# Performance work log

Hardware: AMD Instinct MI355X
Metric: run time of the kernel (lower is better)

## Reference

```python
import jax, jax.numpy as jnp
import numpy as np

HEIGHT, WIDTH = 480, 640
IN_CHANNEL, OUT_CHANNEL, FILTER = 6, 32, 3
B, N = 8, 16384
X_COL, Y_COL, P_COL = 1, 2, 3


def setup_inputs() -> dict:
    key = jax.random.key(0)
    k1, k2, k3, k4 = jax.random.split(key, 4)
    xytp = jax.random.uniform(k1, (B, N, 4), dtype=jnp.float32)
    features = jax.random.normal(k2, (B, N, IN_CHANNEL), dtype=jnp.float32)
    fan_in = FILTER * FILTER * (IN_CHANNEL + 2)
    W = jax.random.normal(k3, (FILTER, FILTER, IN_CHANNEL + 2, OUT_CHANNEL), dtype=jnp.float32) / jnp.sqrt(jnp.float32(fan_in))
    bias = jax.random.normal(k4, (OUT_CHANNEL,), dtype=jnp.float32) * 0.05
    return {"xytp": xytp, "features": features, "W": W, "bias": bias}


def reference(xytp, features, W, bias):
    Bc, Nc = xytp.shape[:2]
    # polarity channels: [pos, neg] concatenated with extra features -> Cin = in_channel + 2
    p = xytp[..., P_COL:P_COL + 1]
    feat = jnp.concatenate([p, 1.0 - p, features], axis=-1)  # [B, N, Cin]
    # event2image: round normalized coords to integer pixel grid (values in [0, H] / [0, W])
    yy = jnp.round(xytp[..., Y_COL] * HEIGHT).astype(jnp.int32)  # [B, N]
    xx = jnp.round(xytp[..., X_COL] * WIDTH).astype(jnp.int32)   # [B, N]
    H1, W1 = HEIGHT + 1, WIDTH + 1
    Cin = feat.shape[-1]
    bidx = jnp.broadcast_to(jnp.arange(Bc)[:, None], (Bc, Nc))
    # scn.InputLayer(mode=3): sum features at duplicate coordinates -> dense scatter-add
    grid = jnp.zeros((Bc, H1, W1, Cin), feat.dtype).at[bidx, yy, xx].add(feat)
    # SubmanifoldConvolution: inactive sites hold zero features, so a dense SAME conv
    # computes the identical gather+GEMM+scatter result at every active site.
    out_grid = jax.lax.conv_general_dilated(
        grid, W, window_strides=(1, 1), padding='SAME',
        dimension_numbers=('NHWC', 'HWIO', 'NHWC')) + bias
    # scn.OutputLayer: each input event reads the feature at its (b, y, x) site
    return out_grid[bidx, yy, xx]  # [B, N, out_channel]
```

## Files before the change

### kernel.cpp

```cpp
#include <hip/hip_runtime.h>
#include <hip/hip_bf16.h>

#define HEIGHT 480
#define WIDTH  640
#define IN_CH  6
#define CIN    8
#define COUT   32
#define BATCH  8
#define NPTS   16384
#define NPTOT  (BATCH * NPTS)
#define GH 483
#define GW 643
#define NCELLS ((size_t)BATCH * GH * GW)
#define NWORDS 77644

__device__ __forceinline__ size_t cell_idx(int b, int gy, int gx) {
    return ((size_t)b * GH + gy) * GW + gx;
}

__device__ __forceinline__ void point_cell(const float4 q, int point,
                                           int& b, int& gy, int& gx) {
    gy = (int)rintf(q.z * (float)HEIGHT) + 1;
    gx = (int)rintf(q.y * (float)WIDTH) + 1;
    b  = point >> 14;
}

__global__ void zero_masks_kernel(uint4* __restrict__ m4, int n4) {
    int i = blockIdx.x * blockDim.x + threadIdx.x;
    if (i < n4) m4[i] = make_uint4(0u, 0u, 0u, 0u);
}

__global__ void count_kernel(const float4* __restrict__ xytp,
                             unsigned int* __restrict__ occ,
                             unsigned int* __restrict__ multi,
                             float* __restrict__ grid) {
    int point = blockIdx.x * blockDim.x + threadIdx.x;
    if (point >= NPTOT) return;
    float4 q = xytp[point];
    int b, gy, gx;
    point_cell(q, point, b, gy, gx);
    size_t ci = cell_idx(b, gy, gx);
    unsigned int word = (unsigned int)(ci >> 5);
    unsigned int bit  = 1u << (ci & 31);
    unsigned int old = atomicOr(&occ[word], bit);
    if (old & bit) {
        atomicOr(&multi[word], bit);
        float* cell = grid + (ci << 3);
        const float4 z = make_float4(0.f, 0.f, 0.f, 0.f);
        *(float4*)(cell)     = z;
        *(float4*)(cell + 4) = z;
    }
}

__global__ void write_kernel(const float4* __restrict__ xytp,
                             const float*  __restrict__ feats,
                             const unsigned int* __restrict__ multi,
                             float* __restrict__ grid) {
    int point = blockIdx.x * blockDim.x + threadIdx.x;
    if (point >= NPTOT) return;
    float4 q = xytp[point];
    int b, gy, gx;
    point_cell(q, point, b, gy, gx);
    size_t ci = cell_idx(b, gy, gx);

    const float* f = feats + (size_t)point * IN_CH;
    float v0 = q.w, v1 = 1.0f - q.w;
    float f0 = f[0], f1 = f[1], f2 = f[2], f3 = f[3], f4 = f[4], f5 = f[5];

    unsigned int word = (unsigned int)(ci >> 5);
    unsigned int bit  = 1u << (ci & 31);

    float* cell = grid + (ci << 3);
    if (!(multi[word] & bit)) {
        *(float4*)(cell)     = make_float4(v0, v1, f0, f1);
        *(float4*)(cell + 4) = make_float4(f2, f3, f4, f5);
    } else {
        unsafeAtomicAdd(cell + 0, v0);
        unsafeAtomicAdd(cell + 1, v1);
        unsafeAtomicAdd(cell + 2, f0);
        unsafeAtomicAdd(cell + 3, f1);
        unsafeAtomicAdd(cell + 4, f2);
        unsafeAtomicAdd(cell + 5, f3);
        unsafeAtomicAdd(cell + 6, f4);
        unsafeAtomicAdd(cell + 7, f5);
    }
}

__global__ void __launch_bounds__(256)
conv_gather_kernel(const float4* __restrict__ xytp,
                   const float*  __restrict__ grid,
                   const unsigned int* __restrict__ occ,
                   const float*  __restrict__ W,
                   const float*  __restrict__ bias,
                   float* __restrict__ out) {
    int tid = blockIdx.x * blockDim.x + threadIdx.x;
    if (tid >= NPTOT * 2) return;
    int point = tid >> 1;
    int sub   = tid & 1;

    float4 q = xytp[point];
    int b, gy, gx;
    point_cell(q, point, b, gy, gx);
    size_t center  = cell_idx(b, gy, gx);
    size_t base_ci = center - GW - 1;

    unsigned int occ9 = 0;
#pragma unroll
    for (int ky = 0; ky < 3; ++ky) {
        size_t ci_row = base_ci + (size_t)ky * GW;
        size_t word = ci_row >> 5;
        int sh = (int)(ci_row & 31);
        unsigned long long two =
            (((unsigned long long)occ[word + 1]) << 32) | occ[word];
        occ9 |= ((unsigned int)(two >> sh) & 7u) << (ky * 3);
    }

    float4 g0[5], g1[5];
#pragma unroll
    for (int k = 0; k < 9; ++k) {
        if ((k & 1) == sub) {
            if (occ9 & (1u << k)) {
                size_t ci = base_ci + (size_t)(k / 3) * GW + (k % 3);
                const float* cell = grid + (ci << 3);
                g0[k >> 1] = *(const float4*)(cell);
                g1[k >> 1] = *(const float4*)(cell + 4);
            }
        }
    }

    float acc[COUT];
#pragma unroll
    for (int c = 0; c < COUT; ++c) acc[c] = sub ? 0.0f : bias[c];

#pragma unroll
    for (int k = 0; k < 9; ++k) {
        if ((k & 1) == sub) {
            if (occ9 & (1u << k)) {
                float4 a = g0[k >> 1], d = g1[k >> 1];
                float gv[CIN] = {a.x, a.y, a.z, a.w, d.x, d.y, d.z, d.w};
                const float* wp = W + k * CIN * COUT;
#pragma unroll
                for (int ci2 = 0; ci2 < CIN; ++ci2) {
#pragma unroll
                    for (int c = 0; c < COUT; ++c) {
                        acc[c] = fmaf(gv[ci2], wp[ci2 * COUT + c], acc[c]);
                    }
                }
            }
        }
    }

    float res[16];
#pragma unroll
    for (int c = 0; c < 16; ++c) {
        float mine  = sub ? acc[16 + c] : acc[c];
        float other = sub ? acc[c]      : acc[16 + c];
        res[c] = mine + __shfl_xor(other, 1);
    }

    float* o = out + (size_t)point * COUT + sub * 16;
#pragma unroll
    for (int c = 0; c < 16; c += 4) {
        *(float4*)(o + c) = make_float4(res[c], res[c + 1], res[c + 2], res[c + 3]);
    }
}

extern "C" void kernel_launch(void* const* d_in, const int* in_sizes, int n_in,
                              void* d_out, int out_size, void* d_ws, size_t ws_size,
                              hipStream_t stream) {
    const float4* xytp  = (const float4*)d_in[0];
    const float*  feats = (const float*)d_in[1];
    const float*  W     = (const float*)d_in[2];
    const float*  bias  = (const float*)d_in[3];
    float* out = (float*)d_out;

    float* grid = (float*)d_ws;
    const size_t grid_bytes = NCELLS * CIN * sizeof(float);
    unsigned int* occ   = (unsigned int*)((char*)d_ws + grid_bytes);
    unsigned int* multi = occ + NWORDS;
    (void)ws_size;

    const int blk = 256;
    const int nblk_pts = (NPTOT + blk - 1) / blk;

    const int n4 = (2 * NWORDS) / 4;
    zero_masks_kernel<<<(n4 + blk - 1) / blk, blk, 0, stream>>>((uint4*)occ, n4);

    count_kernel<<<nblk_pts, blk, 0, stream>>>(xytp, occ, multi, grid);

    write_kernel<<<nblk_pts, blk, 0, stream>>>(xytp, feats, multi, grid);

    conv_gather_kernel<<<nblk_pts * 2, blk, 0, stream>>>(xytp, grid, occ, W, bias, out);
}
```

Before: 45.98 us.

## Store scatter grid as packed bf16 and process two points per thread

The dense scatter grid now stores each cell's 8 input channels as packed bf16 in one 16-byte uint4 instead of 32 bytes of fp32. This halves the bytes written by the scatter and read by the 3x3 gather, and duplicate cells are summed with a CAS loop on bf16 pairs. The count and write kernels also handle two points per thread. The cost is reduced feature precision, since sums are rounded to bf16 at each step, which may exceed the accuracy tolerance. CAS loops on contended cells are also slower than native float atomics.

```diff
diff --git a/kernel.cpp b/kernel.cpp
--- a/kernel.cpp
+++ b/kernel.cpp
@@ -25,6 +25,27 @@
     b  = point >> 14;
 }
 
+__device__ __forceinline__ unsigned int pack_bf16x2(float a, float b) {
+    union { __hip_bfloat162 h; unsigned int u; } cv;
+    cv.h = __float22bfloat162_rn(make_float2(a, b));
+    return cv.u;
+}
+__device__ __forceinline__ float bflo(unsigned int u) {
+    return __uint_as_float(u << 16);
+}
+__device__ __forceinline__ float bfhi(unsigned int u) {
+    return __uint_as_float(u & 0xffff0000u);
+}
+
+__device__ __forceinline__ void cas_add_bf16x2(unsigned int* addr, float a, float b) {
+    unsigned int oldv = *addr, assumed;
+    do {
+        assumed = oldv;
+        unsigned int nv = pack_bf16x2(bflo(assumed) + a, bfhi(assumed) + b);
+        oldv = atomicCAS(addr, assumed, nv);
+    } while (oldv != assumed);
+}
+
 __global__ void zero_masks_kernel(uint4* __restrict__ m4, int n4) {
     int i = blockIdx.x * blockDim.x + threadIdx.x;
     if (i < n4) m4[i] = make_uint4(0u, 0u, 0u, 0u);
@@ -33,62 +54,58 @@
 __global__ void count_kernel(const float4* __restrict__ xytp,
                              unsigned int* __restrict__ occ,
                              unsigned int* __restrict__ multi,
-                             float* __restrict__ grid) {
-    int point = blockIdx.x * blockDim.x + threadIdx.x;
-    if (point >= NPTOT) return;
-    float4 q = xytp[point];
-    int b, gy, gx;
-    point_cell(q, point, b, gy, gx);
-    size_t ci = cell_idx(b, gy, gx);
-    unsigned int word = (unsigned int)(ci >> 5);
-    unsigned int bit  = 1u << (ci & 31);
-    unsigned int old = atomicOr(&occ[word], bit);
-    if (old & bit) {
-        atomicOr(&multi[word], bit);
-        float* cell = grid + (ci << 3);
-        const float4 z = make_float4(0.f, 0.f, 0.f, 0.f);
-        *(float4*)(cell)     = z;
-        *(float4*)(cell + 4) = z;
-    }
+                             uint4* __restrict__ grid) {
+    int t = blockIdx.x * blockDim.x + threadIdx.x;
+    int p0 = t, p1 = t + NPTOT / 2;
+    float4 q0 = xytp[p0];
+    float4 q1 = xytp[p1];
+    int b0, gy0, gx0, b1, gy1, gx1;
+    point_cell(q0, p0, b0, gy0, gx0);
+    point_cell(q1, p1, b1, gy1, gx1);
+    size_t ci0 = cell_idx(b0, gy0, gx0);
+    size_t ci1 = cell_idx(b1, gy1, gx1);
+    unsigned int w0 = (unsigned int)(ci0 >> 5), bit0 = 1u << (ci0 & 31);
+    unsigned int w1 = (unsigned int)(ci1 >> 5), bit1 = 1u << (ci1 & 31);
+    unsigned int old0 = atomicOr(&occ[w0], bit0);
+    unsigned int old1 = atomicOr(&occ[w1], bit1);
+    const uint4 z = make_uint4(0u, 0u, 0u, 0u);
+    if (old0 & bit0) { atomicOr(&multi[w0], bit0); grid[ci0] = z; }
+    if (old1 & bit1) { atomicOr(&multi[w1], bit1); grid[ci1] = z; }
 }
 
 __global__ void write_kernel(const float4* __restrict__ xytp,
                              const float*  __restrict__ feats,
                              const unsigned int* __restrict__ multi,
-                             float* __restrict__ grid) {
-    int point = blockIdx.x * blockDim.x + threadIdx.x;
-    if (point >= NPTOT) return;
-    float4 q = xytp[point];
-    int b, gy, gx;
-    point_cell(q, point, b, gy, gx);
-    size_t ci = cell_idx(b, gy, gx);
-
-    const float* f = feats + (size_t)point * IN_CH;
-    float v0 = q.w, v1 = 1.0f - q.w;
-    float f0 = f[0], f1 = f[1], f2 = f[2], f3 = f[3], f4 = f[4], f5 = f[5];
-
-    unsigned int word = (unsigned int)(ci >> 5);
-    unsigned int bit  = 1u << (ci & 31);
-
-    float* cell = grid + (ci << 3);
-    if (!(multi[word] & bit)) {
-        *(float4*)(cell)     = make_float4(v0, v1, f0, f1);
-        *(float4*)(cell + 4) = make_float4(f2, f3, f4, f5);
-    } else {
-        unsafeAtomicAdd(cell + 0, v0);
-        unsafeAtomicAdd(cell + 1, v1);
-        unsafeAtomicAdd(cell + 2, f0);
-        unsafeAtomicAdd(cell + 3, f1);
-        unsafeAtomicAdd(cell + 4, f2);
-        unsafeAtomicAdd(cell + 5, f3);
-        unsafeAtomicAdd(cell + 6, f4);
-        unsafeAtomicAdd(cell + 7, f5);
+                             uint4* __restrict__ grid) {
+    int t = blockIdx.x * blockDim.x + threadIdx.x;
+#pragma unroll
+    for (int h = 0; h < 2; ++h) {
+        int p = t + h * (NPTOT / 2);
+        float4 q = xytp[p];
+        int b, gy, gx;
+        point_cell(q, p, b, gy, gx);
+        size_t ci = cell_idx(b, gy, gx);
+        const float* f = feats + (size_t)p * IN_CH;
+        float f0 = f[0], f1 = f[1], f2 = f[2], f3 = f[3], f4 = f[4], f5 = f[5];
+        float v0 = q.w, v1 = 1.0f - q.w;
+        unsigned int word = (unsigned int)(ci >> 5);
+        unsigned int bit  = 1u << (ci & 31);
+        if (!(multi[word] & bit)) {
+            grid[ci] = make_uint4(pack_bf16x2(v0, v1), pack_bf16x2(f0, f1),
+                                  pack_bf16x2(f2, f3), pack_bf16x2(f4, f5));
+        } else {
+            unsigned int* cw = (unsigned int*)&grid[ci];
+            cas_add_bf16x2(cw + 0, v0, v1);
+            cas_add_bf16x2(cw + 1, f0, f1);
+            cas_add_bf16x2(cw + 2, f2, f3);
+            cas_add_bf16x2(cw + 3, f4, f5);
+        }
     }
 }
 
 __global__ void __launch_bounds__(256)
 conv_gather_kernel(const float4* __restrict__ xytp,
-                   const float*  __restrict__ grid,
+                   const uint4*  __restrict__ grid,
                    const unsigned int* __restrict__ occ,
                    const float*  __restrict__ W,
                    const float*  __restrict__ bias,
@@ -115,15 +132,13 @@
         occ9 |= ((unsigned int)(two >> sh) & 7u) << (ky * 3);
     }
 
-    float4 g0[5], g1[5];
+    uint4 gc[5];
 #pragma unroll
     for (int k = 0; k < 9; ++k) {
         if ((k & 1) == sub) {
             if (occ9 & (1u << k)) {
                 size_t ci = base_ci + (size_t)(k / 3) * GW + (k % 3);
-                const float* cell = grid + (ci << 3);
-                g0[k >> 1] = *(const float4*)(cell);
-                g1[k >> 1] = *(const float4*)(cell + 4);
+                gc[k >> 1] = grid[ci];
             }
         }
     }
@@ -136,8 +151,9 @@
     for (int k = 0; k < 9; ++k) {
         if ((k & 1) == sub) {
             if (occ9 & (1u << k)) {
-                float4 a = g0[k >> 1], d = g1[k >> 1];
-                float gv[CIN] = {a.x, a.y, a.z, a.w, d.x, d.y, d.z, d.w};
+                uint4 u = gc[k >> 1];
+                float gv[CIN] = {bflo(u.x), bfhi(u.x), bflo(u.y), bfhi(u.y),
+                                 bflo(u.z), bfhi(u.z), bflo(u.w), bfhi(u.w)};
                 const float* wp = W + k * CIN * COUT;
 #pragma unroll
                 for (int ci2 = 0; ci2 < CIN; ++ci2) {
@@ -174,21 +190,20 @@
     const float*  bias  = (const float*)d_in[3];
     float* out = (float*)d_out;
 
-    float* grid = (float*)d_ws;
-    const size_t grid_bytes = NCELLS * CIN * sizeof(float);
+    uint4* grid = (uint4*)d_ws;
+    const size_t grid_bytes = NCELLS * 16;
     unsigned int* occ   = (unsigned int*)((char*)d_ws + grid_bytes);
     unsigned int* multi = occ + NWORDS;
     (void)ws_size;
 
     const int blk = 256;
-    const int nblk_pts = (NPTOT + blk - 1) / blk;
 
     const int n4 = (2 * NWORDS) / 4;
     zero_masks_kernel<<<(n4 + blk - 1) / blk, blk, 0, stream>>>((uint4*)occ, n4);
 
-    count_kernel<<<nblk_pts, blk, 0, stream>>>(xytp, occ, multi, grid);
-
-    write_kernel<<<nblk_pts, blk, 0, stream>>>(xytp, feats, multi, grid);
-
-    conv_gather_kernel<<<nblk_pts * 2, blk, 0, stream>>>(xytp, grid, occ, W, bias, out);
-}
+    count_kernel<<<(NPTOT / 2) / blk, blk, 0, stream>>>(xytp, occ, multi, grid);
+
+    write_kernel<<<(NPTOT / 2) / blk, blk, 0, stream>>>(xytp, feats, multi, grid);
+
+    conv_gather_kernel<<<(NPTOT * 2) / blk, blk, 0, stream>>>(xytp, grid, occ, W, bias, out);
+}
```

New measurement: 50.61 us. 10.1% more time.

## Split conv gather across four threads per point and use nontemporal grid stores

Applied to the files above, without the earlier changes.

The conv gather kernel now assigns four threads per point instead of two. Each thread handles at most three of the nine 3x3 taps, and the partial sums are reduced with a two-level shuffle butterfly. Each thread then writes 8 output channels. This is meant to raise parallelism and cut the serial FMA chain per thread, at the cost of more threads, redundant coordinate and occupancy loads, and extra shuffles. The write kernel also switches its single-event grid stores to nontemporal stores, which risks missing in cache when the conv kernel gathers the same cells shortly after.

```diff
diff --git a/kernel.cpp b/kernel.cpp
--- a/kernel.cpp
+++ b/kernel.cpp
@@ -13,6 +13,8 @@
 #define GW 643
 #define NCELLS ((size_t)BATCH * GH * GW)
 #define NWORDS 77644
+
+typedef float vfloat4 __attribute__((ext_vector_type(4)));
 
 __device__ __forceinline__ size_t cell_idx(int b, int gy, int gx) {
     return ((size_t)b * GH + gy) * GW + gx;
@@ -72,8 +74,10 @@
 
     float* cell = grid + (ci << 3);
     if (!(multi[word] & bit)) {
-        *(float4*)(cell)     = make_float4(v0, v1, f0, f1);
-        *(float4*)(cell + 4) = make_float4(f2, f3, f4, f5);
+        vfloat4 a = {v0, v1, f0, f1};
+        vfloat4 d = {f2, f3, f4, f5};
+        __builtin_nontemporal_store(a, (vfloat4*)cell);
+        __builtin_nontemporal_store(d, (vfloat4*)(cell + 4));
     } else {
         unsafeAtomicAdd(cell + 0, v0);
         unsafeAtomicAdd(cell + 1, v1);
@@ -94,9 +98,8 @@
                    const float*  __restrict__ bias,
                    float* __restrict__ out) {
     int tid = blockIdx.x * blockDim.x + threadIdx.x;
-    if (tid >= NPTOT * 2) return;
-    int point = tid >> 1;
-    int sub   = tid & 1;
+    int point = tid >> 2;
+    int sub   = tid & 3;
 
     float4 q = xytp[point];
     int b, gy, gx;
@@ -115,54 +118,58 @@
         occ9 |= ((unsigned int)(two >> sh) & 7u) << (ky * 3);
     }
 
-    float4 g0[5], g1[5];
-#pragma unroll
-    for (int k = 0; k < 9; ++k) {
-        if ((k & 1) == sub) {
-            if (occ9 & (1u << k)) {
-                size_t ci = base_ci + (size_t)(k / 3) * GW + (k % 3);
-                const float* cell = grid + (ci << 3);
-                g0[k >> 1] = *(const float4*)(cell);
-                g1[k >> 1] = *(const float4*)(cell + 4);
-            }
+    float4 g0[3], g1[3];
+#pragma unroll
+    for (int s = 0; s < 3; ++s) {
+        int k = sub + 4 * s;
+        if (k < 9 && (occ9 & (1u << k))) {
+            size_t ci = base_ci + (size_t)(k / 3) * GW + (k % 3);
+            const float* cell = grid + (ci << 3);
+            g0[s] = *(const float4*)(cell);
+            g1[s] = *(const float4*)(cell + 4);
         }
     }
 
     float acc[COUT];
 #pragma unroll
-    for (int c = 0; c < COUT; ++c) acc[c] = sub ? 0.0f : bias[c];
-
-#pragma unroll
-    for (int k = 0; k < 9; ++k) {
-        if ((k & 1) == sub) {
-            if (occ9 & (1u << k)) {
-                float4 a = g0[k >> 1], d = g1[k >> 1];
-                float gv[CIN] = {a.x, a.y, a.z, a.w, d.x, d.y, d.z, d.w};
-                const float* wp = W + k * CIN * COUT;
-#pragma unroll
-                for (int ci2 = 0; ci2 < CIN; ++ci2) {
-#pragma unroll
-                    for (int c = 0; c < COUT; ++c) {
-                        acc[c] = fmaf(gv[ci2], wp[ci2 * COUT + c], acc[c]);
-                    }
+    for (int c = 0; c < COUT; ++c) acc[c] = (sub == 0) ? bias[c] : 0.0f;
+
+#pragma unroll
+    for (int s = 0; s < 3; ++s) {
+        int k = sub + 4 * s;
+        if (k < 9 && (occ9 & (1u << k))) {
+            float4 a = g0[s], d = g1[s];
+            float gv[CIN] = {a.x, a.y, a.z, a.w, d.x, d.y, d.z, d.w};
+            const float* wp = W + k * CIN * COUT;
+#pragma unroll
+            for (int ci2 = 0; ci2 < CIN; ++ci2) {
+#pragma unroll
+                for (int c = 0; c < COUT; ++c) {
+                    acc[c] = fmaf(gv[ci2], wp[ci2 * COUT + c], acc[c]);
                 }
             }
         }
     }
 
-    float res[16];
+    float h[16];
 #pragma unroll
     for (int c = 0; c < 16; ++c) {
-        float mine  = sub ? acc[16 + c] : acc[c];
-        float other = sub ? acc[c]      : acc[16 + c];
-        res[c] = mine + __shfl_xor(other, 1);
-    }
-
-    float* o = out + (size_t)point * COUT + sub * 16;
-#pragma unroll
-    for (int c = 0; c < 16; c += 4) {
-        *(float4*)(o + c) = make_float4(res[c], res[c + 1], res[c + 2], res[c + 3]);
-    }
+        float mine  = (sub & 1) ? acc[16 + c] : acc[c];
+        float other = (sub & 1) ? acc[c]      : acc[16 + c];
+        h[c] = mine + __shfl_xor(other, 1);
+    }
+    float r[8];
+#pragma unroll
+    for (int c = 0; c < 8; ++c) {
+        float mine  = (sub & 2) ? h[8 + c] : h[c];
+        float other = (sub & 2) ? h[c]     : h[8 + c];
+        r[c] = mine + __shfl_xor(other, 2);
+    }
+
+    int cbase = (sub & 1) * 16 + (sub & 2) * 4;
+    float* o = out + (size_t)point * COUT + cbase;
+    *(float4*)(o)     = make_float4(r[0], r[1], r[2], r[3]);
+    *(float4*)(o + 4) = make_float4(r[4], r[5], r[6], r[7]);
 }
 
 extern "C" void kernel_launch(void* const* d_in, const int* in_sizes, int n_in,
@@ -190,5 +197,5 @@
 
     write_kernel<<<nblk_pts, blk, 0, stream>>>(xytp, feats, multi, grid);
 
-    conv_gather_kernel<<<nblk_pts * 2, blk, 0, stream>>>(xytp, grid, occ, W, bias, out);
-}
+    conv_gather_kernel<<<(NPTOT * 4) / blk, blk, 0, stream>>>(xytp, grid, occ, W, bias, out);
+}
```

Result: slower. 66.77 us (+45.2%).

## Use one thread per point in conv, 64-bit occupancy masks, nontemporal grid stores

Applied to the files above, without the earlier changes.

The conv gather kernel now gives each point a single thread that computes all 9 taps and all 32 outputs, instead of splitting the taps between two lanes and combining them with a shuffle. The occupancy and multi-hit bitmasks switch to 64-bit words, so the 3-cell row window needs a second word only near word boundaries. Single-occupancy grid writes use nontemporal stores. The per-thread work is doubled and more registers are needed (9 float4 pairs plus 32 accumulators), which can lower occupancy and reduces parallelism over 131K points.

```diff
diff --git a/kernel.cpp b/kernel.cpp
--- a/kernel.cpp
+++ b/kernel.cpp
@@ -12,7 +12,9 @@
 #define GH 483
 #define GW 643
 #define NCELLS ((size_t)BATCH * GH * GW)
-#define NWORDS 77644
+#define NW64   38824
+
+typedef float vfloat4 __attribute__((ext_vector_type(4)));
 
 __device__ __forceinline__ size_t cell_idx(int b, int gy, int gx) {
     return ((size_t)b * GH + gy) * GW + gx;
@@ -31,8 +33,8 @@
 }
 
 __global__ void count_kernel(const float4* __restrict__ xytp,
-                             unsigned int* __restrict__ occ,
-                             unsigned int* __restrict__ multi,
+                             unsigned long long* __restrict__ occ,
+                             unsigned long long* __restrict__ multi,
                              float* __restrict__ grid) {
     int point = blockIdx.x * blockDim.x + threadIdx.x;
     if (point >= NPTOT) return;
@@ -40,9 +42,9 @@
     int b, gy, gx;
     point_cell(q, point, b, gy, gx);
     size_t ci = cell_idx(b, gy, gx);
-    unsigned int word = (unsigned int)(ci >> 5);
-    unsigned int bit  = 1u << (ci & 31);
-    unsigned int old = atomicOr(&occ[word], bit);
+    size_t word = ci >> 6;
+    unsigned long long bit = 1ull << (ci & 63);
+    unsigned long long old = atomicOr(&occ[word], bit);
     if (old & bit) {
         atomicOr(&multi[word], bit);
         float* cell = grid + (ci << 3);
@@ -54,7 +56,7 @@
 
 __global__ void write_kernel(const float4* __restrict__ xytp,
                              const float*  __restrict__ feats,
-                             const unsigned int* __restrict__ multi,
+                             const unsigned long long* __restrict__ multi,
                              float* __restrict__ grid) {
     int point = blockIdx.x * blockDim.x + threadIdx.x;
     if (point >= NPTOT) return;
@@ -67,13 +69,12 @@
     float v0 = q.w, v1 = 1.0f - q.w;
     float f0 = f[0], f1 = f[1], f2 = f[2], f3 = f[3], f4 = f[4], f5 = f[5];
 
-    unsigned int word = (unsigned int)(ci >> 5);
-    unsigned int bit  = 1u << (ci & 31);
-
     float* cell = grid + (ci << 3);
-    if (!(multi[word] & bit)) {
-        *(float4*)(cell)     = make_float4(v0, v1, f0, f1);
-        *(float4*)(cell + 4) = make_float4(f2, f3, f4, f5);
+    if (!((multi[ci >> 6] >> (ci & 63)) & 1ull)) {
+        vfloat4 a = {v0, v1, f0, f1};
+        vfloat4 d = {f2, f3, f4, f5};
+        __builtin_nontemporal_store(a, (vfloat4*)cell);
+        __builtin_nontemporal_store(d, (vfloat4*)(cell + 4));
     } else {
         unsafeAtomicAdd(cell + 0, v0);
         unsafeAtomicAdd(cell + 1, v1);
@@ -89,15 +90,12 @@
 __global__ void __launch_bounds__(256)
 conv_gather_kernel(const float4* __restrict__ xytp,
                    const float*  __restrict__ grid,
-                   const unsigned int* __restrict__ occ,
+                   const unsigned long long* __restrict__ occ,
                    const float*  __restrict__ W,
                    const float*  __restrict__ bias,
                    float* __restrict__ out) {
-    int tid = blockIdx.x * blockDim.x + threadIdx.x;
-    if (tid >= NPTOT * 2) return;
-    int point = tid >> 1;
-    int sub   = tid & 1;
-
+    int point = blockIdx.x * blockDim.x + threadIdx.x;
+    if (point >= NPTOT) return;
     float4 q = xytp[point];
     int b, gy, gx;
     point_cell(q, point, b, gy, gx);
@@ -108,60 +106,48 @@
 #pragma unroll
     for (int ky = 0; ky < 3; ++ky) {
         size_t ci_row = base_ci + (size_t)ky * GW;
-        size_t word = ci_row >> 5;
-        int sh = (int)(ci_row & 31);
-        unsigned long long two =
-            (((unsigned long long)occ[word + 1]) << 32) | occ[word];
-        occ9 |= ((unsigned int)(two >> sh) & 7u) << (ky * 3);
+        size_t w  = ci_row >> 6;
+        int    sh = (int)(ci_row & 63);
+        unsigned long long v = occ[w] >> sh;
+        if (sh >= 62) v |= occ[w + 1] << (64 - sh);
+        occ9 |= ((unsigned int)v & 7u) << (ky * 3);
     }
 
-    float4 g0[5], g1[5];
+    float4 g0[9], g1[9];
 #pragma unroll
     for (int k = 0; k < 9; ++k) {
-        if ((k & 1) == sub) {
-            if (occ9 & (1u << k)) {
-                size_t ci = base_ci + (size_t)(k / 3) * GW + (k % 3);
-                const float* cell = grid + (ci << 3);
-                g0[k >> 1] = *(const float4*)(cell);
-                g1[k >> 1] = *(const float4*)(cell + 4);
-            }
+        if (occ9 & (1u << k)) {
+            size_t ci = base_ci + (size_t)(k / 3) * GW + (k % 3);
+            const float* cell = grid + (ci << 3);
+            g0[k] = *(const float4*)(cell);
+            g1[k] = *(const float4*)(cell + 4);
         }
     }
 
     float acc[COUT];
 #pragma unroll
-    for (int c = 0; c < COUT; ++c) acc[c] = sub ? 0.0f : bias[c];
+    for (int c = 0; c < COUT; ++c) acc[c] = bias[c];
 
 #pragma unroll
     for (int k = 0; k < 9; ++k) {
-        if ((k & 1) == sub) {
-            if (occ9 & (1u << k)) {
-                float4 a = g0[k >> 1], d = g1[k >> 1];
-                float gv[CIN] = {a.x, a.y, a.z, a.w, d.x, d.y, d.z, d.w};
-                const float* wp = W + k * CIN * COUT;
+        if (occ9 & (1u << k)) {
+            float4 a = g0[k], d = g1[k];
+            float gv[CIN] = {a.x, a.y, a.z, a.w, d.x, d.y, d.z, d.w};
+            const float* wp = W + k * CIN * COUT;
 #pragma unroll
-                for (int ci2 = 0; ci2 < CIN; ++ci2) {
+            for (int ci2 = 0; ci2 < CIN; ++ci2) {
 #pragma unroll
-                    for (int c = 0; c < COUT; ++c) {
-                        acc[c] = fmaf(gv[ci2], wp[ci2 * COUT + c], acc[c]);
-                    }
+                for (int c = 0; c < COUT; ++c) {
+                    acc[c] = fmaf(gv[ci2], wp[ci2 * COUT + c], acc[c]);
                 }
             }
         }
     }
 
-    float res[16];
+    float* o = out + (size_t)point * COUT;
 #pragma unroll
-    for (int c = 0; c < 16; ++c) {
-        float mine  = sub ? acc[16 + c] : acc[c];
-        float other = sub ? acc[c]      : acc[16 + c];
-        res[c] = mine + __shfl_xor(other, 1);
-    }
-
-    float* o = out + (size_t)point * COUT + sub * 16;
-#pragma unroll
-    for (int c = 0; c < 16; c += 4) {
-        *(float4*)(o + c) = make_float4(res[c], res[c + 1], res[c + 2], res[c + 3]);
+    for (int c = 0; c < COUT; c += 4) {
+        *(float4*)(o + c) = make_float4(acc[c], acc[c + 1], acc[c + 2], acc[c + 3]);
     }
 }
 
@@ -176,19 +162,19 @@
 
     float* grid = (float*)d_ws;
     const size_t grid_bytes = NCELLS * CIN * sizeof(float);
-    unsigned int* occ   = (unsigned int*)((char*)d_ws + grid_bytes);
-    unsigned int* multi = occ + NWORDS;
+    unsigned long long* occ   = (unsigned long long*)((char*)d_ws + grid_bytes);
+    unsigned long long* multi = occ + NW64;
     (void)ws_size;
 
     const int blk = 256;
     const int nblk_pts = (NPTOT + blk - 1) / blk;
 
-    const int n4 = (2 * NWORDS) / 4;
+    const int n4 = (2 * NW64 * 8) / 16;
     zero_masks_kernel<<<(n4 + blk - 1) / blk, blk, 0, stream>>>((uint4*)occ, n4);
 
     count_kernel<<<nblk_pts, blk, 0, stream>>>(xytp, occ, multi, grid);
 
     write_kernel<<<nblk_pts, blk, 0, stream>>>(xytp, feats, multi, grid);
 
-    conv_gather_kernel<<<nblk_pts * 2, blk, 0, stream>>>(xytp, grid, occ, W, bias, out);
+    conv_gather_kernel<<<nblk_pts, blk, 0, stream>>>(xytp, grid, occ, W, bias, out);
 }
```

New measurement: 41.95 us. 1.1x faster.
